# Kernel tuning notes

Hardware: AMD Instinct MI355X
Metric: run time of the kernel (lower is better)

## Reference

```python
import jax, jax.numpy as jnp
import numpy as np

EMBED = 1024
HIDDEN = 1024

def setup_inputs() -> dict:
    key = jax.random.key(0)
    k1, k2, k3, k4, k5 = jax.random.split(key, 5)
    B, T = 32, 512
    s_ih = 1.0 / np.sqrt(HIDDEN)
    x = jax.random.normal(k1, (B, T, EMBED), dtype=jnp.float32)
    # PyTorch nn.RNN params: W_ih [H,E], W_hh [H,H], b_ih [H], b_hh [H], init U(-1/sqrt(H), 1/sqrt(H))
    W_ih = jax.random.uniform(k2, (HIDDEN, EMBED), minval=-s_ih, maxval=s_ih, dtype=jnp.float32)
    W_hh = jax.random.uniform(k3, (HIDDEN, HIDDEN), minval=-s_ih, maxval=s_ih, dtype=jnp.float32)
    b_ih = jax.random.uniform(k4, (HIDDEN,), minval=-s_ih, maxval=s_ih, dtype=jnp.float32)
    b_hh = jax.random.uniform(k5, (HIDDEN,), minval=-s_ih, maxval=s_ih, dtype=jnp.float32)
    return {"x": x, "W_ih": W_ih, "W_hh": W_hh, "b_ih": b_ih, "b_hh": b_hh}

def reference(x, W_ih, W_hh, b_ih, b_hh):
    # h_t = tanh(x_t @ W_ih^T + b_ih + h_{t-1} @ W_hh^T + b_hh), h_0 = 0
    B, T, E = x.shape
    H = W_hh.shape[0]
    # Precompute the input projection for all timesteps in one big GEMM.
    xp = jnp.einsum('bte,he->bth', x, W_ih) + (b_ih + b_hh)  # [B,T,H]
    h0 = jnp.zeros((B, H), dtype=x.dtype)

    def step(h, xp_t):
        h_new = jnp.tanh(xp_t + h @ W_hh.T)
        return h_new, h_new

    _, outs = jax.lax.scan(step, h0, jnp.swapaxes(xp, 0, 1))  # outs: [T,B,H]
    return jnp.swapaxes(outs, 0, 1)  # [B,T,H]
```

## Files before the change

kernel.cpp:

```cpp
#include <hip/hip_runtime.h>
#include <stdint.h>

#define B_ 32
#define T_ 512
#define E_ 1024
#define H_ 1024
#define NWAVE 64

typedef __attribute__((ext_vector_type(8))) short short8;
typedef __attribute__((ext_vector_type(4))) float floatx4;

__device__ __forceinline__ unsigned short bf16_of(float f) {
    unsigned u = __float_as_uint(f);
    return (unsigned short)((u + 0x8000u) >> 16);
}

__device__ __forceinline__ short8 load_bf8(const float* __restrict__ p) {
    const float4* q = (const float4*)p;
    float4 v0 = q[0];
    float4 v1 = q[1];
    short8 r;
    r[0] = (short)bf16_of(v0.x); r[1] = (short)bf16_of(v0.y);
    r[2] = (short)bf16_of(v0.z); r[3] = (short)bf16_of(v0.w);
    r[4] = (short)bf16_of(v1.x); r[5] = (short)bf16_of(v1.y);
    r[6] = (short)bf16_of(v1.z); r[7] = (short)bf16_of(v1.w);
    return r;
}

__global__ __launch_bounds__(256) void k_xp(const float* __restrict__ x,
                                            const float* __restrict__ Wih,
                                            const float* __restrict__ bih,
                                            const float* __restrict__ bhh,
                                            float* __restrict__ out) {
    const int tid  = threadIdx.x;
    const int w    = tid >> 6;
    const int lane = tid & 63;
    const int l15  = lane & 15;
    const int quad = lane >> 4;
    const int rb = blockIdx.x & 127;
    const int cb = blockIdx.x >> 7;
    const int row_base = rb * 128 + w * 32;
    const int col_base = cb * 128;

    floatx4 acc[2][8];
#pragma unroll
    for (int i = 0; i < 2; i++)
#pragma unroll
        for (int j = 0; j < 8; j++) acc[i][j] = (floatx4)0.0f;

    for (int k0 = 0; k0 < E_; k0 += 32) {
        const int koff = k0 + quad * 8;
        short8 a[2];
#pragma unroll
        for (int mt = 0; mt < 2; mt++)
            a[mt] = load_bf8(x + (size_t)(row_base + mt * 16 + l15) * E_ + koff);
        short8 b[8];
#pragma unroll
        for (int nt = 0; nt < 8; nt++)
            b[nt] = load_bf8(Wih + (size_t)(col_base + nt * 16 + l15) * E_ + koff);
#pragma unroll
        for (int mt = 0; mt < 2; mt++)
#pragma unroll
            for (int nt = 0; nt < 8; nt++)
                acc[mt][nt] = __builtin_amdgcn_mfma_f32_16x16x32_bf16(
                    a[mt], b[nt], acc[mt][nt], 0, 0, 0);
    }

#pragma unroll
    for (int nt = 0; nt < 8; nt++) {
        const int col = col_base + nt * 16 + l15;
        const float bias = bih[col] + bhh[col];
#pragma unroll
        for (int mt = 0; mt < 2; mt++) {
            const int row = row_base + mt * 16 + quad * 4;
#pragma unroll
            for (int r = 0; r < 4; r++)
                out[(size_t)(row + r) * H_ + col] = acc[mt][nt][r] + bias;
        }
    }
}

__global__ void k_init(unsigned* __restrict__ ws) {
    const int i = blockIdx.x * blockDim.x + threadIdx.x;
    if (i < 33792) ws[i] = 0u;
}

__global__ __launch_bounds__(64, 1) void k_rnn(const float* __restrict__ Whh,
                                               float* __restrict__ out,
                                               unsigned* __restrict__ ws) {
    const int lane = threadIdx.x;
    const int l15  = lane & 15;
    const int quad = lane >> 4;
    const int wid  = blockIdx.x;
    const int j0   = wid * 16;

    unsigned short* hb    = (unsigned short*)ws;
    unsigned*       flags = ws + 32768;

    short8 wreg[32];
#pragma unroll
    for (int c = 0; c < 32; c++)
        wreg[c] = load_bf8(Whh + (size_t)(j0 + l15) * H_ + c * 32 + quad * 8);

#pragma unroll 1
    for (int t = 0; t < T_; t++) {
        const unsigned short* cur = hb + (size_t)(t & 1) * (B_ * H_);
        unsigned short*       nxt = hb + (size_t)((t + 1) & 1) * (B_ * H_);

        float xv[2][4];
#pragma unroll
        for (int mt = 0; mt < 2; mt++)
#pragma unroll
            for (int r = 0; r < 4; r++) {
                const int b = mt * 16 + quad * 4 + r;
                xv[mt][r] = out[((size_t)b * T_ + t) * H_ + j0 + l15];
            }

        if (t > 0) {
            const unsigned tv = (unsigned)t;
            while (true) {
                unsigned v = __hip_atomic_load(&flags[lane * 16], __ATOMIC_RELAXED,
                                               __HIP_MEMORY_SCOPE_AGENT);
                if (__ballot(v < tv) == 0ull) break;
            }
            __builtin_amdgcn_fence(__ATOMIC_ACQUIRE, "agent");
        }

        floatx4 acc[2];
        acc[0] = (floatx4)0.0f;
        acc[1] = (floatx4)0.0f;
#pragma unroll
        for (int c = 0; c < 32; c++) {
#pragma unroll
            for (int mt = 0; mt < 2; mt++) {
                short8 ah = *(const short8*)(cur + (size_t)(mt * 16 + l15) * H_ +
                                             c * 32 + quad * 8);
                acc[mt] = __builtin_amdgcn_mfma_f32_16x16x32_bf16(ah, wreg[c],
                                                                  acc[mt], 0, 0, 0);
            }
        }

#pragma unroll
        for (int mt = 0; mt < 2; mt++) {
#pragma unroll
            for (int r = 0; r < 4; r++) {
                const int b = mt * 16 + quad * 4 + r;
                const float p = xv[mt][r] + acc[mt][r];
                const float h = 1.0f - 2.0f / (__expf(2.0f * p) + 1.0f);
                out[((size_t)b * T_ + t) * H_ + j0 + l15] = h;
                const unsigned short hu = bf16_of(h);
                const unsigned short pu =
                    (unsigned short)__shfl_xor((int)hu, 1, 64);
                if ((l15 & 1) == 0) {
                    const unsigned packed = (unsigned)hu | ((unsigned)pu << 16);
                    __hip_atomic_store(
                        (unsigned*)(nxt + (size_t)b * H_ + j0 + l15), packed,
                        __ATOMIC_RELAXED, __HIP_MEMORY_SCOPE_AGENT);
                }
            }
        }

        asm volatile("s_waitcnt vmcnt(0)" ::: "memory");
        if (lane == 0)
            __hip_atomic_store(&flags[wid * 16], (unsigned)(t + 1),
                               __ATOMIC_RELAXED, __HIP_MEMORY_SCOPE_AGENT);
    }
}

extern "C" void kernel_launch(void* const* d_in, const int* in_sizes, int n_in,
                              void* d_out, int out_size, void* d_ws, size_t ws_size,
                              hipStream_t stream) {
    const float* x   = (const float*)d_in[0];
    const float* Wih = (const float*)d_in[1];
    const float* Whh = (const float*)d_in[2];
    const float* bih = (const float*)d_in[3];
    const float* bhh = (const float*)d_in[4];
    float* out = (float*)d_out;
    unsigned* ws = (unsigned*)d_ws;

    k_init<<<132, 256, 0, stream>>>(ws);
    k_xp<<<128 * 8, 256, 0, stream>>>(x, Wih, bih, bhh, out);
    k_rnn<<<NWAVE, 64, 0, stream>>>(Whh, out, ws);
}
```

Baseline: 2.640 ms.

## Store hidden state in MFMA-fragment order and publish flag before output writes

The bf16 hidden-state buffer is rewritten in a fragment-major layout. Each lane now reads its A operand as one contiguous short8 indexed by (c, mt, lane), giving fully coalesced loads in the serial recurrence. Results are staged through LDS and written as 16-byte chunks per lane, replacing the shuffle-and-pair stores. The fp32 output stores move after the step flag is set, so other waves can proceed without waiting on those writes. The price is an LDS round trip each step and reliance on implicit wave-level LDS ordering with no barrier, which holds only because the block is a single wavefront.

Measured after the change: 3.323 ms. +25.9%, slower.

```diff
diff --git a/kernel.cpp b/kernel.cpp
--- a/kernel.cpp
+++ b/kernel.cpp
@@ -9,6 +9,7 @@
 
 typedef __attribute__((ext_vector_type(8))) short short8;
 typedef __attribute__((ext_vector_type(4))) float floatx4;
+typedef __attribute__((ext_vector_type(4))) int int4v;
 
 __device__ __forceinline__ unsigned short bf16_of(float f) {
     unsigned u = __float_as_uint(f);
@@ -97,6 +98,14 @@
     unsigned short* hb    = (unsigned short*)ws;
     unsigned*       flags = ws + 32768;
 
+    const int mt_s = lane >> 5;
+    const int sub  = (lane >> 4) & 1;
+    const int m_s  = lane & 15;
+    const int slot = (wid >> 1) * 128 + mt_s * 64 + (wid & 1) * 32 + sub * 16 + m_s;
+    const int lds_off = mt_s * 512 + m_s * 32 + sub * 16;
+
+    __shared__ unsigned short sh[512];
+
     short8 wreg[32];
 #pragma unroll
     for (int c = 0; c < 32; c++)
@@ -104,8 +113,8 @@
 
 #pragma unroll 1
     for (int t = 0; t < T_; t++) {
-        const unsigned short* cur = hb + (size_t)(t & 1) * (B_ * H_);
-        unsigned short*       nxt = hb + (size_t)((t + 1) & 1) * (B_ * H_);
+        const short8* hc = (const short8*)(hb + (size_t)(t & 1) * (B_ * H_));
+        unsigned*     nx = (unsigned*)(hb + (size_t)((t + 1) & 1) * (B_ * H_));
 
         float xv[2][4];
 #pragma unroll
@@ -133,37 +142,41 @@
         for (int c = 0; c < 32; c++) {
 #pragma unroll
             for (int mt = 0; mt < 2; mt++) {
-                short8 ah = *(const short8*)(cur + (size_t)(mt * 16 + l15) * H_ +
-                                             c * 32 + quad * 8);
+                short8 ah = hc[(c * 2 + mt) * 64 + lane];
                 acc[mt] = __builtin_amdgcn_mfma_f32_16x16x32_bf16(ah, wreg[c],
                                                                   acc[mt], 0, 0, 0);
             }
         }
 
+        float hv[2][4];
 #pragma unroll
-        for (int mt = 0; mt < 2; mt++) {
+        for (int mt = 0; mt < 2; mt++)
 #pragma unroll
             for (int r = 0; r < 4; r++) {
-                const int b = mt * 16 + quad * 4 + r;
                 const float p = xv[mt][r] + acc[mt][r];
                 const float h = 1.0f - 2.0f / (__expf(2.0f * p) + 1.0f);
-                out[((size_t)b * T_ + t) * H_ + j0 + l15] = h;
-                const unsigned short hu = bf16_of(h);
-                const unsigned short pu =
-                    (unsigned short)__shfl_xor((int)hu, 1, 64);
-                if ((l15 & 1) == 0) {
-                    const unsigned packed = (unsigned)hu | ((unsigned)pu << 16);
-                    __hip_atomic_store(
-                        (unsigned*)(nxt + (size_t)b * H_ + j0 + l15), packed,
-                        __ATOMIC_RELAXED, __HIP_MEMORY_SCOPE_AGENT);
-                }
+                hv[mt][r] = h;
+                sh[(mt * 16 + quad * 4 + r) * 16 + l15] = bf16_of(h);
             }
-        }
+
+        int4v tv4 = *(const int4v*)((const char*)sh + lds_off);
+#pragma unroll
+        for (int i = 0; i < 4; i++)
+            __hip_atomic_store(nx + slot * 4 + i, ((unsigned*)&tv4)[i],
+                               __ATOMIC_RELAXED, __HIP_MEMORY_SCOPE_AGENT);
 
         asm volatile("s_waitcnt vmcnt(0)" ::: "memory");
         if (lane == 0)
             __hip_atomic_store(&flags[wid * 16], (unsigned)(t + 1),
                                __ATOMIC_RELAXED, __HIP_MEMORY_SCOPE_AGENT);
+
+#pragma unroll
+        for (int mt = 0; mt < 2; mt++)
+#pragma unroll
+            for (int r = 0; r < 4; r++) {
+                const int b = mt * 16 + quad * 4 + r;
+                out[((size_t)b * T_ + t) * H_ + j0 + l15] = hv[mt][r];
+            }
     }
 }
 
```
